# Kernel optimization log

Hardware: AMD Instinct MI355X
Metric: run time of the kernel (lower is better)

## Reference

```python
import jax, jax.numpy as jnp
import numpy as np

D = 1024      # model dim
DH = 64       # dim_head
H = 8         # heads
INNER = DH * H
L = 6         # depth
NL = 64       # num_latents
MF = 128      # max_num_frames
FF = 4 * D    # ff_mult * dim
B, T, F, V = 4, 8, 4, 256


def _ln(x, g, b):
    m = x.mean(-1, keepdims=True)
    v = x.var(-1, keepdims=True)
    return (x - m) / jnp.sqrt(v + 1e-5) * g + b


def setup_inputs() -> dict:
    key = jax.random.key(0)
    ks = jax.random.split(key, 8)
    s = 0.02
    x = jax.random.normal(ks[0], (B, T, F, V, D), jnp.float32)
    latents = jax.random.normal(ks[1], (NL, D), jnp.float32)
    frame_embs = jax.random.normal(ks[2], (MF, D), jnp.float32)
    Wq = jax.random.normal(ks[3], (L, D, INNER), jnp.float32) * s
    Wkv = jax.random.normal(ks[4], (L, D, 2 * INNER), jnp.float32) * s
    Wo = jax.random.normal(ks[5], (L, INNER, D), jnp.float32) * s
    W1 = jax.random.normal(ks[6], (L, D, FF), jnp.float32) * s
    W2 = jax.random.normal(ks[7], (L, FF, D), jnp.float32) * s
    ones = jnp.ones((L, D), jnp.float32)
    zeros = jnp.zeros((L, D), jnp.float32)
    return dict(
        x=x, latents=latents, frame_embs=frame_embs,
        g_media=ones, b_media=zeros, g_lat=ones, b_lat=zeros,
        Wq=Wq, Wkv=Wkv, Wo=Wo, g_ff=ones, b_ff=zeros, W1=W1, W2=W2,
        g_out=jnp.ones((D,), jnp.float32), b_out=jnp.zeros((D,), jnp.float32),
    )


def reference(x, latents, frame_embs, g_media, b_media, g_lat, b_lat,
              Wq, Wkv, Wo, g_ff, b_ff, W1, W2, g_out, b_out):
    scale = DH ** -0.5
    # add frame embeddings (indexed by T, as in original code), merge F,v dims
    x = x + frame_embs[:T][None, :, None, None, :]
    x = x.reshape(B, T, F * V, D)
    lat0 = jnp.broadcast_to(latents, (B, T, NL, D))

    def split_heads(a):  # (b, t, n, h*d) -> (b, h, t, n, d)
        return a.reshape(B, T, -1, H, DH).transpose(0, 3, 1, 2, 4)

    def block(lat, p):
        gm, bm, gl, bl, wq, wkv, wo, gf, bf, w1, w2 = p
        xm = _ln(x, gm, bm)
        ln_l = _ln(lat, gl, bl)
        q = (ln_l @ wq) * scale
        kv = jnp.concatenate([xm, ln_l], axis=-2) @ wkv
        k, v = jnp.split(kv, 2, axis=-1)
        q, k, v = split_heads(q), split_heads(k), split_heads(v)
        sim = jnp.einsum('bhtid,bhtjd->bhtij', q, k)
        attn = jax.nn.softmax(sim, axis=-1)
        o = jnp.einsum('bhtij,bhtjd->bhtid', attn, v)
        o = o.transpose(0, 2, 3, 1, 4).reshape(B, T, NL, INNER)
        lat = o @ wo + lat
        ff = jax.nn.gelu(_ln(lat, gf, bf) @ w1, approximate=False) @ w2
        return lat + ff, None

    lat, _ = jax.lax.scan(block, lat0,
                          (g_media, b_media, g_lat, b_lat, Wq, Wkv, Wo,
                           g_ff, b_ff, W1, W2))
    return _ln(lat, g_out, b_out)
```

## Files before the change

### kernel.cpp

```cpp
#include <hip/hip_runtime.h>
#include <math.h>

#define D_      1024
#define DH_     64
#define H_      8
#define INNER_  512
#define L_      6
#define NL_     64
#define FF_     4096
#define B_      4
#define T_      8
#define FV_     1024
#define BT_     32
#define MROWS_  32768
#define NKV_    1088
#define KVROWS_ 34816
#define ZB_     256

typedef __bf16 bf16;
typedef __bf16 bf16x8 __attribute__((ext_vector_type(8)));
typedef __bf16 bf16x4 __attribute__((ext_vector_type(4)));
typedef float  f32x4  __attribute__((ext_vector_type(4)));

#define BARRIER() { asm volatile("" ::: "memory"); __builtin_amdgcn_s_barrier(); asm volatile("" ::: "memory"); }
#define ENDPH() { __builtin_amdgcn_sched_barrier(0); asm volatile("s_waitcnt lgkmcnt(0)"); __builtin_amdgcn_sched_barrier(0); BARRIER(); }

__device__ __forceinline__ void gload_lds16(const bf16* g, bf16* l) {
    __builtin_amdgcn_global_load_lds(
        (const __attribute__((address_space(1))) unsigned int*)g,
        (__attribute__((address_space(3))) unsigned int*)l, 16, 0, 0);
}

__device__ __forceinline__ float wred_sum(float v) {
#pragma unroll
    for (int o = 32; o > 0; o >>= 1) v += __shfl_xor(v, o, 64);
    return v;
}

__device__ __forceinline__ float gelu_f(float x) {
    return 0.5f * x * (1.0f + erff(x * 0.70710678118654752440f));
}

__global__ __launch_bounds__(256) void xhat_k(const float* __restrict__ x,
                                              const float* __restrict__ fe,
                                              bf16* __restrict__ xhat) {
    __shared__ float red[8];
    int row = blockIdx.x;
    int t = (row >> 10) & 7;
    const float* xr = x + (size_t)row * D_;
    const float* fr_ = fe + (size_t)t * D_;
    int tid = threadIdx.x, c = tid * 4;
    float4 v = *(const float4*)(xr + c);
    float4 f = *(const float4*)(fr_ + c);
    v.x += f.x; v.y += f.y; v.z += f.z; v.w += f.w;
    float s = v.x + v.y + v.z + v.w;
    float ss = v.x * v.x + v.y * v.y + v.z * v.z + v.w * v.w;
    s = wred_sum(s); ss = wred_sum(ss);
    if ((tid & 63) == 0) { red[tid >> 6] = s; red[4 + (tid >> 6)] = ss; }
    __syncthreads();
    s = red[0] + red[1] + red[2] + red[3];
    ss = red[4] + red[5] + red[6] + red[7];
    float mean = s * (1.0f / D_);
    float rstd = rsqrtf(ss * (1.0f / D_) - mean * mean + 1e-5f);
    bf16x4 o;
    o[0] = (bf16)((v.x - mean) * rstd);
    o[1] = (bf16)((v.y - mean) * rstd);
    o[2] = (bf16)((v.z - mean) * rstd);
    o[3] = (bf16)((v.w - mean) * rstd);
    *(bf16x4*)(xhat + (size_t)row * D_ + c) = o;
}

__global__ __launch_bounds__(256) void latinit_k(const float* __restrict__ latents,
                                                 float* __restrict__ lat) {
    int row = blockIdx.x;
    int i = row & 63;
    int c = threadIdx.x * 4;
    float4 v = *(const float4*)(latents + (size_t)i * D_ + c);
    *(float4*)(lat + (size_t)row * D_ + c) = v;
}

template<int OUTF>
__global__ __launch_bounds__(256) void ln_k(const float* __restrict__ in,
                                            const float* __restrict__ g,
                                            const float* __restrict__ b,
                                            void* __restrict__ out) {
    __shared__ float red[8];
    int row = blockIdx.x;
    const float* x = in + (size_t)row * D_;
    int tid = threadIdx.x, c = tid * 4;
    float4 v = *(const float4*)(x + c);
    float s = v.x + v.y + v.z + v.w;
    float ss = v.x * v.x + v.y * v.y + v.z * v.z + v.w * v.w;
    s = wred_sum(s); ss = wred_sum(ss);
    if ((tid & 63) == 0) { red[tid >> 6] = s; red[4 + (tid >> 6)] = ss; }
    __syncthreads();
    s = red[0] + red[1] + red[2] + red[3];
    ss = red[4] + red[5] + red[6] + red[7];
    float mean = s * (1.0f / D_);
    float rstd = rsqrtf(ss * (1.0f / D_) - mean * mean + 1e-5f);
    float4 gv = *(const float4*)(g + c);
    float4 bv = *(const float4*)(b + c);
    float o0 = (v.x - mean) * rstd * gv.x + bv.x;
    float o1 = (v.y - mean) * rstd * gv.y + bv.y;
    float o2 = (v.z - mean) * rstd * gv.z + bv.z;
    float o3 = (v.w - mean) * rstd * gv.w + bv.w;
    if (OUTF) {
        *(float4*)((float*)out + (size_t)row * D_ + c) = make_float4(o0, o1, o2, o3);
    } else {
        bf16x4 o; o[0] = (bf16)o0; o[1] = (bf16)o1; o[2] = (bf16)o2; o[3] = (bf16)o3;
        *(bf16x4*)((bf16*)out + (size_t)row * D_ + c) = o;
    }
}

template<int NP, int OUTF>
__global__ __launch_bounds__(256) void accln_k(float* __restrict__ lat,
                                               const float* __restrict__ p, long long s,
                                               const float* __restrict__ g,
                                               const float* __restrict__ b,
                                               void* __restrict__ out) {
    __shared__ float red[8];
    int row = blockIdx.x;
    int tid = threadIdx.x, c = tid * 4;
    float* lr = lat + (size_t)row * D_;
    float4 a = *(const float4*)(lr + c);
#pragma unroll
    for (int w = 0; w < NP; w++) {
        float4 x = *(const float4*)(p + (size_t)w * s + (size_t)row * D_ + c);
        a.x += x.x; a.y += x.y; a.z += x.z; a.w += x.w;
    }
    if (!OUTF) *(float4*)(lr + c) = a;
    float sm = a.x + a.y + a.z + a.w;
    float ss = a.x * a.x + a.y * a.y + a.z * a.z + a.w * a.w;
    sm = wred_sum(sm); ss = wred_sum(ss);
    if ((tid & 63) == 0) { red[tid >> 6] = sm; red[4 + (tid >> 6)] = ss; }
    __syncthreads();
    sm = red[0] + red[1] + red[2] + red[3];
    ss = red[4] + red[5] + red[6] + red[7];
    float mean = sm * (1.0f / D_);
    float rstd = rsqrtf(ss * (1.0f / D_) - mean * mean + 1e-5f);
    float4 gv = *(const float4*)(g + c);
    float4 bv = *(const float4*)(b + c);
    float o0 = (a.x - mean) * rstd * gv.x + bv.x;
    float o1 = (a.y - mean) * rstd * gv.y + bv.y;
    float o2 = (a.z - mean) * rstd * gv.z + bv.z;
    float o3 = (a.w - mean) * rstd * gv.w + bv.w;
    if (OUTF) {
        *(float4*)((float*)out + (size_t)row * D_ + c) = make_float4(o0, o1, o2, o3);
    } else {
        bf16x4 o; o[0] = (bf16)o0; o[1] = (bf16)o1; o[2] = (bf16)o2; o[3] = (bf16)o3;
        *(bf16x4*)((bf16*)out + (size_t)row * D_ + c) = o;
    }
}

__device__ __forceinline__ void wt_tile(const float* __restrict__ in, int R, int C,
                                        bf16* __restrict__ out, int bx, int by,
                                        const float* __restrict__ sc,
                                        const float* __restrict__ bm,
                                        float* __restrict__ bkv) {
    __shared__ float t[32][33];
    int c0 = bx * 32, r0 = by * 32;
    int tx = threadIdx.x & 31, ty = threadIdx.x >> 5;
#pragma unroll
    for (int i = 0; i < 4; i++)
        t[ty + i * 8][tx] = in[(size_t)(r0 + ty + i * 8) * C + c0 + tx];
    __syncthreads();
    float scale = sc ? sc[r0 + tx] : 1.0f;
#pragma unroll
    for (int i = 0; i < 4; i++)
        out[(size_t)(c0 + ty + i * 8) * R + r0 + tx] = (bf16)(t[tx][ty + i * 8] * scale);
    if (bm && ty == 0) {
        float s = 0.0f;
#pragma unroll
        for (int r = 0; r < 32; r++) s += bm[r0 + r] * t[r][tx];
        atomicAdd(&bkv[c0 + tx], s);
    }
}

__global__ __launch_bounds__(256) void wprep_k(const float* __restrict__ wq,
                                               const float* __restrict__ wkv,
                                               const float* __restrict__ wo,
                                               const float* __restrict__ w1,
                                               const float* __restrict__ w2,
                                               const float* __restrict__ gm,
                                               const float* __restrict__ bm,
                                               float* __restrict__ bkv,
                                               bf16* __restrict__ BcatQ,
                                               bf16* __restrict__ BcatKV,
                                               bf16* __restrict__ WkvTg,
                                               bf16* __restrict__ WoT,
                                               bf16* __restrict__ W1T,
                                               bf16* __restrict__ W2T) {
    int id = blockIdx.x;
    if (id < 512)            wt_tile(wq, D_, INNER_, BcatQ, id & 15, id >> 4, nullptr, nullptr, nullptr);
    else if (id < 1536)  { int i = id - 512;  wt_tile(wkv, D_, 2 * INNER_, BcatKV, i & 31, i >> 5, nullptr, nullptr, nullptr); }
    else if (id < 2560)  { int i = id - 1536; wt_tile(wkv, D_, 2 * INNER_, WkvTg, i & 31, i >> 5, gm, bm, bkv); }
    else if (id < 3072)  { int i = id - 2560; wt_tile(wo, INNER_, D_, WoT, i & 31, i >> 5, nullptr, nullptr, nullptr); }
    else if (id < 7168)  { int i = id - 3072; wt_tile(w1, D_, FF_, W1T, i & 127, i >> 7, nullptr, nullptr, nullptr); }
    else                 { int i = id - 7168; wt_tile(w2, FF_, D_, W2T, i & 31, i >> 5, nullptr, nullptr, nullptr); }
}

__global__ __launch_bounds__(512, 1) void gemm_kv(const bf16* __restrict__ Ag,
                                                  const bf16* __restrict__ Bg,
                                                  bf16* __restrict__ KVb,
                                                  bf16* __restrict__ vt,
                                                  const float* __restrict__ bias) {
    __shared__ bf16 lds[2][32768];
    const int lda = D_, ldb = D_;
    const int tid = threadIdx.x;
    const int w = tid >> 6, lane = tid & 63;
    const int wm = w >> 2, wn = w & 3;
    const size_t m0 = (size_t)blockIdx.x * 256;
    const size_t n0 = (size_t)blockIdx.y * 256;
    const int nt = 16;

    const int p0 = (w * 2) * 64 + lane, p1 = p0 + 64;
    const int sr0 = p0 >> 3, sk0 = ((p0 & 7) ^ (sr0 & 7)) * 8;
    const int sr1 = p1 >> 3, sk1 = ((p1 & 7) ^ (sr1 & 7)) * 8;
    const int scw0 = (w * 2) * 512, scw1 = scw0 + 512;

    auto STAGE = [&](const bf16* g, int ld, size_t row0, int k0, bf16* bufb, int rb) {
        gload_lds16(g + (row0 + sr0) * (size_t)ld + k0 + sk0, bufb + rb + scw0);
        gload_lds16(g + (row0 + sr1) * (size_t)ld + k0 + sk1, bufb + rb + scw1);
    };

    const int fr = lane & 15;
    const int pK0 = (((lane >> 4)) ^ (fr & 7)) * 8;
    const int pK1 = ((4 + (lane >> 4)) ^ (fr & 7)) * 8;
    const size_t aoff = (size_t)(wm * 128 + fr) * 64;
    const size_t boff = 16384 + (size_t)(wn * 64 + fr) * 64;

    f32x4 acc[8][4];
#pragma unroll
    for (int i = 0; i < 8; i++)
#pragma unroll
        for (int j = 0; j < 4; j++)
#pragma unroll
            for (int r = 0; r < 4; r++) acc[i][j][r] = 0.0f;

    bf16x8 aX[4], aY[4], bA[4][2], bB[4][2];

    auto LDA2 = [&](const bf16* lb, int i0, bf16x8 (&d)[4]) {
        d[0] = *(const bf16x8*)(lb + aoff + (size_t)i0 * 1024 + pK0);
        d[1] = *(const bf16x8*)(lb + aoff + (size_t)i0 * 1024 + pK1);
        d[2] = *(const bf16x8*)(lb + aoff + (size_t)(i0 + 1) * 1024 + pK0);
        d[3] = *(const bf16x8*)(lb + aoff + (size_t)(i0 + 1) * 1024 + pK1);
    };
    auto LDB8 = [&](const bf16* lb, bf16x8 (&bb)[4][2]) {
#pragma unroll
        for (int j = 0; j < 4; j++) {
            bb[j][0] = *(const bf16x8*)(lb + boff + j * 1024 + pK0);
            bb[j][1] = *(const bf16x8*)(lb + boff + j * 1024 + pK1);
        }
    };
    auto MM2 = [&](int i0, bf16x8 (&a)[4], bf16x8 (&bb)[4][2]) {
        __builtin_amdgcn_s_setprio(1);
#pragma unroll
        for (int j = 0; j < 4; j++) {
            acc[i0][j]     = __builtin_amdgcn_mfma_f32_16x16x32_bf16(a[0], bb[j][0], acc[i0][j], 0, 0, 0);
            acc[i0][j]     = __builtin_amdgcn_mfma_f32_16x16x32_bf16(a[1], bb[j][1], acc[i0][j], 0, 0, 0);
            acc[i0 + 1][j] = __builtin_amdgcn_mfma_f32_16x16x32_bf16(a[2], bb[j][0], acc[i0 + 1][j], 0, 0, 0);
            acc[i0 + 1][j] = __builtin_amdgcn_mfma_f32_16x16x32_bf16(a[3], bb[j][1], acc[i0 + 1][j], 0, 0, 0);
        }
        __builtin_amdgcn_s_setprio(0);
    };

    STAGE(Bg, ldb, n0,       0, lds[0], 16384);
    STAGE(Bg, ldb, n0 + 128, 0, lds[0], 24576);
    STAGE(Ag, lda, m0,       0, lds[0], 0);
    STAGE(Ag, lda, m0 + 128, 0, lds[0], 8192);
    STAGE(Bg, ldb, n0,       64, lds[1], 16384);
    STAGE(Bg, ldb, n0 + 128, 64, lds[1], 24576);
    STAGE(Ag, lda, m0,       64, lds[1], 0);
    asm volatile("s_waitcnt vmcnt(6)");
    BARRIER();
    LDB8(lds[0], bA);
    LDA2(lds[0], 0, aX);

    auto tile4 = [&](const bf16* lb, bf16* lbn, bf16x8 (&BU)[4][2], bf16x8 (&BL)[4][2], int t) {
        bf16* lbw = (bf16*)lb;
        LDA2(lb, 2, aY);
        if (t + 1 < nt) STAGE(Ag, lda, m0 + 128, (t + 1) << 6, lbn, 8192);
        MM2(0, aX, BU);
        ENDPH();
        LDA2(lb, 4, aX);
        if (t + 2 < nt) STAGE(Bg, ldb, n0, (t + 2) << 6, lbw, 16384);
        MM2(2, aY, BU);
        ENDPH();
        LDA2(lb, 6, aY);
        if (t + 2 < nt) STAGE(Bg, ldb, n0 + 128, (t + 2) << 6, lbw, 24576);
        MM2(4, aX, BU);
        __builtin_amdgcn_sched_barrier(0);
        asm volatile("s_waitcnt lgkmcnt(0)");
        __builtin_amdgcn_sched_barrier(0);
        if (t < nt - 2)       { asm volatile("s_waitcnt vmcnt(4)"); }
        else if (t == nt - 2) { asm volatile("s_waitcnt vmcnt(0)"); }
        BARRIER();
        if (t + 1 < nt) { LDB8(lbn, BL); LDA2(lbn, 0, aX); }
        if (t + 2 < nt) STAGE(Ag, lda, m0, (t + 2) << 6, lbw, 0);
        MM2(6, aY, BU);
        ENDPH();
    };

    for (int t = 0; t < nt; t += 2) {
        tile4(lds[0], lds[1], bA, bB, t);
        tile4(lds[1], lds[0], bB, bA, t + 1);
    }

    const int fq = (lane >> 4) * 4;
#pragma unroll
    for (int i = 0; i < 8; i++)
#pragma unroll
        for (int j = 0; j < 4; j++) {
            size_t cb = n0 + wn * 64 + j * 16 + fr;
            float bv = bias[cb];
            size_t mb = m0 + wm * 128 + i * 16 + fq;
            if (cb < 512) {
#pragma unroll
                for (int r = 0; r < 4; r++) {
                    size_t m = mb + r;
                    size_t rb = m + ((m >> 10) << 6);
                    KVb[rb * 512 + cb] = (bf16)(acc[i][j][r] + bv);
                }
            } else {
                int hh = ((int)cb - 512) >> 6, dh = ((int)cb - 512) & 63;
                size_t bt = mb >> 10, jl = mb & 1023;
                bf16x4 v4;
#pragma unroll
                for (int r = 0; r < 4; r++) v4[r] = (bf16)(acc[i][j][r] + bv);
                *(bf16x4*)(vt + ((bt * 8 + hh) * 64 + dh) * (size_t)NKV_ + jl) = v4;
            }
        }
}

template<int MODE>
__global__ __launch_bounds__(512, 1) void gemm_ff(const bf16* __restrict__ Ag, int lda,
                                                  const bf16* __restrict__ Bg, int ldb,
                                                  void* __restrict__ C, int ldc,
                                                  int K, long long czs) {
    __shared__ bf16 lds[2][24576];
    const int tid = threadIdx.x;
    const int w = tid >> 6, lane = tid & 63;
    const int wm = w >> 2, wn = w & 3;
    const size_t m0 = (size_t)blockIdx.x * 128;
    const size_t n0 = (size_t)blockIdx.y * 256;
    const int klen = K / gridDim.z;
    const int koff = blockIdx.z * klen;
    const int nt = klen >> 6;

    const int p0 = (w * 2) * 64 + lane, p1 = p0 + 64;
    const int sr0 = p0 >> 3, sk0 = ((p0 & 7) ^ (sr0 & 7)) * 8;
    const int sr1 = p1 >> 3, sk1 = ((p1 & 7) ^ (sr1 & 7)) * 8;
    const int scw0 = (w * 2) * 512, scw1 = scw0 + 512;

    auto STAGE = [&](const bf16* g, int ld, size_t row0, int k0, bf16* bufb, int rb) {
        gload_lds16(g + (row0 + sr0) * (size_t)ld + k0 + sk0, bufb + rb + scw0);
        gload_lds16(g + (row0 + sr1) * (size_t)ld + k0 + sk1, bufb + rb + scw1);
    };

    const int fr = lane & 15;
    const int pK0 = (((lane >> 4)) ^ (fr & 7)) * 8;
    const int pK1 = ((4 + (lane >> 4)) ^ (fr & 7)) * 8;
    const size_t aoff = (size_t)(wm * 64 + fr) * 64;
    const size_t boff = 8192 + (size_t)(wn * 64 + fr) * 64;

    f32x4 acc[4][4];
#pragma unroll
    for (int i = 0; i < 4; i++)
#pragma unroll
        for (int j = 0; j < 4; j++)
#pragma unroll
            for (int r = 0; r < 4; r++) acc[i][j][r] = 0.0f;

    bf16x8 aX[2], aY[2], bA[4][2], bB[4][2];

    auto LDA1 = [&](const bf16* lb, int i0, bf16x8 (&d)[2]) {
        d[0] = *(const bf16x8*)(lb + aoff + (size_t)i0 * 1024 + pK0);
        d[1] = *(const bf16x8*)(lb + aoff + (size_t)i0 * 1024 + pK1);
    };
    auto LDB8 = [&](const bf16* lb, bf16x8 (&bb)[4][2]) {
#pragma unroll
        for (int j = 0; j < 4; j++) {
            bb[j][0] = *(const bf16x8*)(lb + boff + j * 1024 + pK0);
            bb[j][1] = *(const bf16x8*)(lb + boff + j * 1024 + pK1);
        }
    };
    auto MM1 = [&](int i0, bf16x8 (&a)[2], bf16x8 (&bb)[4][2]) {
        __builtin_amdgcn_s_setprio(1);
#pragma unroll
        for (int j = 0; j < 4; j++) {
            acc[i0][j] = __builtin_amdgcn_mfma_f32_16x16x32_bf16(a[0], bb[j][0], acc[i0][j], 0, 0, 0);
            acc[i0][j] = __builtin_amdgcn_mfma_f32_16x16x32_bf16(a[1], bb[j][1], acc[i0][j], 0, 0, 0);
        }
        __builtin_amdgcn_s_setprio(0);
    };

    STAGE(Ag, lda, m0,       koff,      lds[0], 0);
    STAGE(Bg, ldb, n0,       koff,      lds[0], 8192);
    STAGE(Bg, ldb, n0 + 128, koff,      lds[0], 16384);
    STAGE(Bg, ldb, n0,       koff + 64, lds[1], 8192);
    STAGE(Bg, ldb, n0 + 128, koff + 64, lds[1], 16384);
    asm volatile("s_waitcnt vmcnt(4)");
    BARRIER();
    LDB8(lds[0], bA);
    LDA1(lds[0], 0, aX);

    auto tile4 = [&](const bf16* lb, bf16* lbn, bf16x8 (&BU)[4][2], bf16x8 (&BL)[4][2], int t) {
        bf16* lbw = (bf16*)lb;
        LDA1(lb, 1, aY);
        if (t + 1 < nt) STAGE(Ag, lda, m0, koff + ((t + 1) << 6), lbn, 0);
        MM1(0, aX, BU);
        ENDPH();
        LDA1(lb, 2, aX);
        if (t + 2 < nt) STAGE(Bg, ldb, n0, koff + ((t + 2) << 6), lbw, 8192);
        MM1(1, aY, BU);
        ENDPH();
        LDA1(lb, 3, aY);
        if (t + 2 < nt) STAGE(Bg, ldb, n0 + 128, koff + ((t + 2) << 6), lbw, 16384);
        MM1(2, aX, BU);
        __builtin_amdgcn_sched_barrier(0);
        asm volatile("s_waitcnt lgkmcnt(0)");
        __builtin_amdgcn_sched_barrier(0);
        if (t < nt - 2)       { asm volatile("s_waitcnt vmcnt(4)"); }
        else if (t == nt - 2) { asm volatile("s_waitcnt vmcnt(0)"); }
        BARRIER();
        if (t + 1 < nt) { LDB8(lbn, BL); LDA1(lbn, 0, aX); }
        MM1(3, aY, BU);
        ENDPH();
    };

    for (int t = 0; t < nt; t += 2) {
        tile4(lds[0], lds[1], bA, bB, t);
        tile4(lds[1], lds[0], bB, bA, t + 1);
    }

    const int fq = (lane >> 4) * 4;
#pragma unroll
    for (int i = 0; i < 4; i++)
#pragma unroll
        for (int j = 0; j < 4; j++) {
            size_t cb = n0 + wn * 64 + j * 16 + fr;
            size_t mb = m0 + wm * 64 + i * 16 + fq;
#pragma unroll
            for (int r = 0; r < 4; r++) {
                float v = acc[i][j][r];
                if (MODE == 4) {
                    ((float*)C + blockIdx.z * czs)[(mb + r) * (size_t)ldc + cb] = v;
                } else {
                    ((bf16*)C)[(mb + r) * (size_t)ldc + cb] = (bf16)gelu_f(v);
                }
            }
        }
}

template<int MODE, int CMAP>
__global__ __launch_bounds__(256) void gemm128(const bf16* __restrict__ A, int lda,
                                               const bf16* __restrict__ Bw, int ldb,
                                               void* __restrict__ C, int ldc,
                                               int K, float scale,
                                               long long czs, void* __restrict__ C2,
                                               void* __restrict__ C3) {
    __shared__ bf16 As[128 * 32];
    __shared__ bf16 Bs[128 * 32];
    const int tid = threadIdx.x;
    const int wave = tid >> 6;
    const int lane = tid & 63;
    const size_t m0 = (size_t)blockIdx.x * 128;
    const size_t n0 = (size_t)blockIdx.y * 128;
    const int wm = (wave >> 1) * 64;
    const int wn = (wave & 1) * 64;

    const int klen = K / gridDim.z;
    const int koff = blockIdx.z * klen;

    const int r0 = tid >> 2;
    const int c0 = ((tid & 3) ^ ((tid >> 3) & 3)) * 8;
    const bf16* ga0 = A + (m0 + r0) * lda + c0 + koff;
    const bf16* ga1 = A + (m0 + r0 + 64) * lda + c0 + koff;
    const bf16* gb0 = Bw + (n0 + r0) * ldb + c0 + koff;
    const bf16* gb1 = Bw + (n0 + r0 + 64) * ldb + c0 + koff;
    bf16* la0 = As + wave * 512;
    bf16* la1 = As + 2048 + wave * 512;
    bf16* lb0 = Bs + wave * 512;
    bf16* lb1 = Bs + 2048 + wave * 512;

    f32x4 acc[4][4];
#pragma unroll
    for (int i = 0; i < 4; i++)
#pragma unroll
        for (int j = 0; j < 4; j++)
#pragma unroll
            for (int r = 0; r < 4; r++) acc[i][j][r] = 0.0f;

    const int fr = lane & 15;
    const int q = lane >> 4;
    const int sw = (q ^ ((fr >> 1) & 3)) * 8;

    for (int kt = 0; kt < klen; kt += 32) {
        gload_lds16(ga0 + kt, la0);
        gload_lds16(ga1 + kt, la1);
        gload_lds16(gb0 + kt, lb0);
        gload_lds16(gb1 + kt, lb1);
        __syncthreads();
        bf16x8 af[4], bfv[4];
#pragma unroll
        for (int i = 0; i < 4; i++) {
            af[i]  = *(const bf16x8*)(As + (wm + i * 16 + fr) * 32 + sw);
            bfv[i] = *(const bf16x8*)(Bs + (wn + i * 16 + fr) * 32 + sw);
        }
#pragma unroll
        for (int i = 0; i < 4; i++)
#pragma unroll
            for (int j = 0; j < 4; j++)
                acc[i][j] = __builtin_amdgcn_mfma_f32_16x16x32_bf16(af[i], bfv[j], acc[i][j], 0, 0, 0);
        __syncthreads();
    }

    const int fq = (lane >> 4) * 4;
#pragma unroll
    for (int i = 0; i < 4; i++)
#pragma unroll
        for (int j = 0; j < 4; j++) {
            size_t cb = n0 + wn + j * 16 + fr;
            size_t mb = m0 + wm + i * 16 + fq;
            if (CMAP == 3) {
                if (cb < 512) {
#pragma unroll
                    for (int r = 0; r < 4; r++)
                        ((bf16*)C)[(mb + r) * 512 + cb] = (bf16)(acc[i][j][r] * scale);
                } else if (cb < 1024) {
#pragma unroll
                    for (int r = 0; r < 4; r++) {
                        size_t m = mb + r;
                        size_t rb = (m >> 6) * (size_t)NKV_ + 1024 + (m & 63);
                        ((bf16*)C2)[rb * 512 + (cb - 512)] = (bf16)acc[i][j][r];
                    }
                } else {
                    int hh = ((int)cb - 1024) >> 6, dh = ((int)cb - 1024) & 63;
                    size_t bt = mb >> 6, jl = 1024 + (mb & 63);
                    bf16x4 v4;
#pragma unroll
                    for (int r = 0; r < 4; r++) v4[r] = (bf16)acc[i][j][r];
                    *(bf16x4*)((bf16*)C3 + ((bt * 8 + hh) * 64 + dh) * (size_t)NKV_ + jl) = v4;
                }
            } else {
#pragma unroll
                for (int r = 0; r < 4; r++) {
                    float v = acc[i][j][r];
                    if (MODE == 4) {
                        ((float*)C + blockIdx.z * czs)[(mb + r) * ldc + cb] = v;
                    } else {
                        ((bf16*)C)[(mb + r) * ldc + cb] = (bf16)v;
                    }
                }
            }
        }
}

__global__ __launch_bounds__(256, 2) void attn_k(const bf16* __restrict__ qb,
                                                 const bf16* __restrict__ KVb,
                                                 const bf16* __restrict__ vt,
                                                 bf16* __restrict__ ob) {
    __shared__ float comb[4][64 * 66];
    __shared__ float sc[4][64];
    __shared__ float mw[4][64], lw[4][64];
    const int z = blockIdx.x, bt = z >> 3, h = z & 7;
    const int tid = threadIdx.x, w = tid >> 6, lane = tid & 63;
    const int fr = lane & 15, g = lane >> 4;
    const bf16* Qz = qb + (size_t)(bt * 64) * INNER_ + h * DH_;
    const bf16* Kz = KVb + (size_t)bt * NKV_ * 512 + h * DH_;
    const bf16* Vz = vt + (size_t)z * (DH_ * NKV_);
    bf16* Pw = (bf16*)(&comb[w][0]);

    bf16x8 qf[4][2];
#pragma unroll
    for (int nj = 0; nj < 4; nj++)
#pragma unroll
        for (int ks = 0; ks < 2; ks++)
            qf[nj][ks] = *(const bf16x8*)(Qz + (size_t)(fr + 16 * nj) * INNER_ + g * 8 + ks * 32);

    f32x4 acc_o[4][4];
#pragma unroll
    for (int i = 0; i < 4; i++)
#pragma unroll
        for (int j = 0; j < 4; j++)
#pragma unroll
            for (int r = 0; r < 4; r++) acc_o[i][j][r] = 0.0f;
    float m_reg[4] = {-INFINITY, -INFINITY, -INFINITY, -INFINITY};
    float l_reg[4] = {0.0f, 0.0f, 0.0f, 0.0f};

    const int nch = (w == 0) ? 5 : 4;
    for (int ci = 0; ci < nch; ci++) {
        const int kc0 = (w + ci * 4) * 64;
        f32x4 s[4][4];
#pragma unroll
        for (int i = 0; i < 4; i++)
#pragma unroll
            for (int j = 0; j < 4; j++)
#pragma unroll
                for (int r = 0; r < 4; r++) s[i][j][r] = 0.0f;
#pragma unroll
        for (int ks = 0; ks < 2; ks++) {
            bf16x8 kf[4];
#pragma unroll
            for (int mi = 0; mi < 4; mi++)
                kf[mi] = *(const bf16x8*)(Kz + (size_t)(kc0 + fr + 16 * mi) * 512 + g * 8 + ks * 32);
#pragma unroll
            for (int mi = 0; mi < 4; mi++)
#pragma unroll
                for (int nj = 0; nj < 4; nj++)
                    s[mi][nj] = __builtin_amdgcn_mfma_f32_16x16x32_bf16(kf[mi], qf[nj][ks], s[mi][nj], 0, 0, 0);
        }
        float pmax[4];
#pragma unroll
        for (int nj = 0; nj < 4; nj++) {
            float mx = s[0][nj][0];
#pragma unroll
            for (int mi = 0; mi < 4; mi++)
#pragma unroll
                for (int r = 0; r < 4; r++) mx = fmaxf(mx, s[mi][nj][r]);
            mx = fmaxf(mx, __shfl_xor(mx, 16, 64));
            mx = fmaxf(mx, __shfl_xor(mx, 32, 64));
            pmax[nj] = mx;
        }
        bool grew = (pmax[0] > m_reg[0]) || (pmax[1] > m_reg[1]) ||
                    (pmax[2] > m_reg[2]) || (pmax[3] > m_reg[3]);
        if (__any(grew ? 1 : 0)) {
            float so[4];
#pragma unroll
            for (int nj = 0; nj < 4; nj++) {
                float mn = fmaxf(m_reg[nj], pmax[nj]);
                so[nj] = __expf(m_reg[nj] - mn);
                m_reg[nj] = mn;
                l_reg[nj] *= so[nj];
            }
            if (g == 0) {
#pragma unroll
                for (int nj = 0; nj < 4; nj++) sc[w][fr + 16 * nj] = so[nj];
            }
            asm volatile("s_waitcnt lgkmcnt(0)" ::: "memory");
#pragma unroll
            for (int mi = 0; mi < 4; mi++)
#pragma unroll
                for (int r = 0; r < 4; r++) {
                    float sq = sc[w][16 * mi + 4 * g + r];
#pragma unroll
                    for (int jd = 0; jd < 4; jd++) acc_o[mi][jd][r] *= sq;
                }
        }
        float psum[4] = {0.0f, 0.0f, 0.0f, 0.0f};
#pragma unroll
        for (int mi = 0; mi < 4; mi++)
#pragma unroll
            for (int nj = 0; nj < 4; nj++) {
                bf16x4 pb4;
#pragma unroll
                for (int r = 0; r < 4; r++) {
                    float pv = __expf(s[mi][nj][r] - m_reg[nj]);
                    psum[nj] += pv;
                    pb4[r] = (bf16)pv;
                }
                *(bf16x4*)(Pw + (size_t)(fr + 16 * nj) * 72 + 16 * mi + 4 * g) = pb4;
            }
#pragma unroll
        for (int nj = 0; nj < 4; nj++) {
            float ps = psum[nj];
            ps += __shfl_xor(ps, 16, 64);
            ps += __shfl_xor(ps, 32, 64);
            l_reg[nj] += ps;
        }
        asm volatile("s_waitcnt lgkmcnt(0)" ::: "memory");
#pragma unroll
        for (int ks = 0; ks < 2; ks++) {
            bf16x8 af[4], vf[4];
#pragma unroll
            for (int mi = 0; mi < 4; mi++)
                af[mi] = *(const bf16x8*)(Pw + (size_t)(fr + 16 * mi) * 72 + g * 8 + ks * 32);
#pragma unroll
            for (int jd = 0; jd < 4; jd++)
                vf[jd] = *(const bf16x8*)(Vz + (size_t)(fr + 16 * jd) * NKV_ + kc0 + g * 8 + ks * 32);
#pragma unroll
            for (int mi = 0; mi < 4; mi++)
#pragma unroll
                for (int jd = 0; jd < 4; jd++)
                    acc_o[mi][jd] = __builtin_amdgcn_mfma_f32_16x16x32_bf16(af[mi], vf[jd], acc_o[mi][jd], 0, 0, 0);
        }
    }

    if (g == 0) {
#pragma unroll
        for (int nj = 0; nj < 4; nj++) {
            mw[w][fr + 16 * nj] = m_reg[nj];
            lw[w][fr + 16 * nj] = l_reg[nj];
        }
    }
    asm volatile("s_waitcnt lgkmcnt(0)" ::: "memory");
#pragma unroll
    for (int mi = 0; mi < 4; mi++)
#pragma unroll
        for (int jd = 0; jd < 4; jd++)
#pragma unroll
            for (int r = 0; r < 4; r++)
                comb[w][(16 * mi + 4 * g + r) * 66 + fr + 16 * jd] = acc_o[mi][jd][r];
    __syncthreads();
    {
        int q = tid >> 2, d0 = (tid & 3) * 16;
        float M = fmaxf(fmaxf(mw[0][q], mw[1][q]), fmaxf(mw[2][q], mw[3][q]));
        float al[4], l = 0.0f;
#pragma unroll
        for (int ww = 0; ww < 4; ww++) { al[ww] = __expf(mw[ww][q] - M); l += al[ww] * lw[ww][q]; }
        float inv = 1.0f / l;
        bf16 outv[16];
#pragma unroll
        for (int dd = 0; dd < 16; dd++) {
            float o = 0.0f;
#pragma unroll
            for (int ww = 0; ww < 4; ww++) o += comb[ww][q * 66 + d0 + dd] * al[ww];
            outv[dd] = (bf16)(o * inv);
        }
        bf16* dst = ob + (size_t)(bt * 64 + q) * INNER_ + h * 64 + d0;
        *(bf16x8*)dst = *(bf16x8*)outv;
        *(bf16x8*)(dst + 8) = *(bf16x8*)(outv + 8);
    }
}

extern "C" void kernel_launch(void* const* d_in, const int* in_sizes, int n_in,
                              void* d_out, int out_size, void* d_ws, size_t ws_size,
                              hipStream_t stream) {
    const float* x       = (const float*)d_in[0];
    const float* latents = (const float*)d_in[1];
    const float* fe      = (const float*)d_in[2];
    const float* g_media = (const float*)d_in[3];
    const float* b_media = (const float*)d_in[4];
    const float* g_lat   = (const float*)d_in[5];
    const float* b_lat   = (const float*)d_in[6];
    const float* Wq      = (const float*)d_in[7];
    const float* Wkv     = (const float*)d_in[8];
    const float* Wo      = (const float*)d_in[9];
    const float* g_ff    = (const float*)d_in[10];
    const float* b_ff    = (const float*)d_in[11];
    const float* W1      = (const float*)d_in[12];
    const float* W2      = (const float*)d_in[13];
    const float* g_out   = (const float*)d_in[14];
    const float* b_out   = (const float*)d_in[15];

    char* p = (char*)d_ws;
    auto alloc = [&](size_t bytes) { char* r = p; p += (bytes + 255) & ~(size_t)255; return r; };
    bf16*  xhat = (bf16*)alloc((size_t)MROWS_ * D_ * 2);
    float* lat  = (float*)alloc((size_t)2048 * D_ * 4);
    bf16*  lnl  = (bf16*)alloc((size_t)2048 * D_ * 2);
    bf16*  qb   = (bf16*)alloc((size_t)2048 * INNER_ * 2);
    bf16*  KVb  = (bf16*)alloc((size_t)KVROWS_ * 512 * 2);
    bf16*  vt   = (bf16*)alloc((size_t)ZB_ * DH_ * NKV_ * 2);
    bf16*  ob   = (bf16*)alloc((size_t)2048 * INNER_ * 2);
    bf16*  Bcat = (bf16*)alloc((size_t)1536 * D_ * 2);
    bf16*  WkvTg= (bf16*)alloc((size_t)D_ * D_ * 2);
    bf16*  WoT  = (bf16*)alloc((size_t)D_ * INNER_ * 2);
    bf16*  W1T  = (bf16*)alloc((size_t)FF_ * D_ * 2);
    bf16*  W2T  = (bf16*)alloc((size_t)D_ * FF_ * 2);
    float* bkv  = (float*)alloc(1024 * 4);
    float* ffp  = (float*)alloc((size_t)4 * 2048 * D_ * 4);
    bf16*  ffh  = vt;

    xhat_k<<<MROWS_, 256, 0, stream>>>(x, fe, xhat);
    latinit_k<<<2048, 256, 0, stream>>>(latents, lat);
    ln_k<0><<<2048, 256, 0, stream>>>(lat, g_lat, b_lat, lnl);

    const long long PS = (long long)2048 * D_;

    for (int l = 0; l < L_; l++) {
        const float* gm = g_media + (size_t)l * D_;
        const float* bm = b_media + (size_t)l * D_;
        const float* gf = g_ff + (size_t)l * D_;
        const float* bf_ = b_ff + (size_t)l * D_;
        const float* wq = Wq + (size_t)l * D_ * INNER_;
        const float* wkv = Wkv + (size_t)l * D_ * 2 * INNER_;
        const float* wo = Wo + (size_t)l * INNER_ * D_;
        const float* w1 = W1 + (size_t)l * D_ * FF_;
        const float* w2 = W2 + (size_t)l * FF_ * D_;

        hipMemsetAsync(bkv, 0, 1024 * 4, stream);
        wprep_k<<<11264, 256, 0, stream>>>(wq, wkv, wo, w1, w2, gm, bm, bkv,
                                           Bcat, Bcat + (size_t)512 * D_, WkvTg, WoT, W1T, W2T);

        gemm_kv<<<dim3(128, 4), 512, 0, stream>>>(xhat, WkvTg, KVb, vt, bkv);
        gemm128<0, 3><<<dim3(16, 12), 256, 0, stream>>>(
            lnl, D_, Bcat, D_, qb, 0, D_, 0.125f, 0, KVb, vt);

        attn_k<<<ZB_, 256, 0, stream>>>(qb, KVb, vt, ob);

        gemm128<4, 0><<<dim3(16, 8, 2), 256, 0, stream>>>(
            ob, INNER_, WoT, INNER_, ffp, D_, INNER_, 1.0f, PS, nullptr, nullptr);
        accln_k<2, 0><<<2048, 256, 0, stream>>>(lat, ffp, PS, gf, bf_, lnl);

        gemm_ff<3><<<dim3(16, 16), 512, 0, stream>>>(
            lnl, D_, W1T, D_, ffh, FF_, D_, 0);
        gemm_ff<4><<<dim3(16, 4, 4), 512, 0, stream>>>(
            ffh, FF_, W2T, FF_, ffp, D_, FF_, PS);
        if (l < L_ - 1) {
            accln_k<4, 0><<<2048, 256, 0, stream>>>(lat, ffp, PS,
                g_lat + (size_t)(l + 1) * D_, b_lat + (size_t)(l + 1) * D_, lnl);
        } else {
            accln_k<4, 1><<<2048, 256, 0, stream>>>(lat, ffp, PS, g_out, b_out, (float*)d_out);
        }
    }
}
```

Measured before the change: 1.324 ms.

## Replace register-prefetched GEMM main loop with per-phase barrier-synchronized schedule

```diff
diff --git a/kernel.cpp b/kernel.cpp
--- a/kernel.cpp
+++ b/kernel.cpp
@@ -237,33 +237,6 @@
 #pragma unroll
             for (int r = 0; r < 4; r++) acc[i][j][r] = 0.0f;
 
-    bf16x8 aX[4], aY[4], bA[4][2], bB[4][2];
-
-    auto LDA2 = [&](const bf16* lb, int i0, bf16x8 (&d)[4]) {
-        d[0] = *(const bf16x8*)(lb + aoff + (size_t)i0 * 1024 + pK0);
-        d[1] = *(const bf16x8*)(lb + aoff + (size_t)i0 * 1024 + pK1);
-        d[2] = *(const bf16x8*)(lb + aoff + (size_t)(i0 + 1) * 1024 + pK0);
-        d[3] = *(const bf16x8*)(lb + aoff + (size_t)(i0 + 1) * 1024 + pK1);
-    };
-    auto LDB8 = [&](const bf16* lb, bf16x8 (&bb)[4][2]) {
-#pragma unroll
-        for (int j = 0; j < 4; j++) {
-            bb[j][0] = *(const bf16x8*)(lb + boff + j * 1024 + pK0);
-            bb[j][1] = *(const bf16x8*)(lb + boff + j * 1024 + pK1);
-        }
-    };
-    auto MM2 = [&](int i0, bf16x8 (&a)[4], bf16x8 (&bb)[4][2]) {
-        __builtin_amdgcn_s_setprio(1);
-#pragma unroll
-        for (int j = 0; j < 4; j++) {
-            acc[i0][j]     = __builtin_amdgcn_mfma_f32_16x16x32_bf16(a[0], bb[j][0], acc[i0][j], 0, 0, 0);
-            acc[i0][j]     = __builtin_amdgcn_mfma_f32_16x16x32_bf16(a[1], bb[j][1], acc[i0][j], 0, 0, 0);
-            acc[i0 + 1][j] = __builtin_amdgcn_mfma_f32_16x16x32_bf16(a[2], bb[j][0], acc[i0 + 1][j], 0, 0, 0);
-            acc[i0 + 1][j] = __builtin_amdgcn_mfma_f32_16x16x32_bf16(a[3], bb[j][1], acc[i0 + 1][j], 0, 0, 0);
-        }
-        __builtin_amdgcn_s_setprio(0);
-    };
-
     STAGE(Bg, ldb, n0,       0, lds[0], 16384);
     STAGE(Bg, ldb, n0 + 128, 0, lds[0], 24576);
     STAGE(Ag, lda, m0,       0, lds[0], 0);
@@ -273,37 +246,97 @@
     STAGE(Ag, lda, m0,       64, lds[1], 0);
     asm volatile("s_waitcnt vmcnt(6)");
     BARRIER();
-    LDB8(lds[0], bA);
-    LDA2(lds[0], 0, aX);
-
-    auto tile4 = [&](const bf16* lb, bf16* lbn, bf16x8 (&BU)[4][2], bf16x8 (&BL)[4][2], int t) {
-        bf16* lbw = (bf16*)lb;
-        LDA2(lb, 2, aY);
-        if (t + 1 < nt) STAGE(Ag, lda, m0 + 128, (t + 1) << 6, lbn, 8192);
-        MM2(0, aX, BU);
-        ENDPH();
-        LDA2(lb, 4, aX);
-        if (t + 2 < nt) STAGE(Bg, ldb, n0, (t + 2) << 6, lbw, 16384);
-        MM2(2, aY, BU);
-        ENDPH();
-        LDA2(lb, 6, aY);
-        if (t + 2 < nt) STAGE(Bg, ldb, n0 + 128, (t + 2) << 6, lbw, 24576);
-        MM2(4, aX, BU);
-        __builtin_amdgcn_sched_barrier(0);
-        asm volatile("s_waitcnt lgkmcnt(0)");
-        __builtin_amdgcn_sched_barrier(0);
-        if (t < nt - 2)       { asm volatile("s_waitcnt vmcnt(4)"); }
-        else if (t == nt - 2) { asm volatile("s_waitcnt vmcnt(0)"); }
-        BARRIER();
-        if (t + 1 < nt) { LDB8(lbn, BL); LDA2(lbn, 0, aX); }
-        if (t + 2 < nt) STAGE(Ag, lda, m0, (t + 2) << 6, lbw, 0);
-        MM2(6, aY, BU);
-        ENDPH();
-    };
-
-    for (int t = 0; t < nt; t += 2) {
-        tile4(lds[0], lds[1], bA, bB, t);
-        tile4(lds[1], lds[0], bB, bA, t + 1);
+
+    for (int t = 0; t < nt; ++t) {
+        const bf16* lb = lds[t & 1];
+        bf16* lbw = lds[t & 1];
+        bf16* lbn = lds[(t + 1) & 1];
+        const int kt1 = (t + 1) << 6, kt2 = (t + 2) << 6;
+        bf16x8 bfr[4][2];
+
+        {
+#pragma unroll
+            for (int j = 0; j < 4; j++) {
+                bfr[j][0] = *(const bf16x8*)(lb + boff + j * 1024 + pK0);
+                bfr[j][1] = *(const bf16x8*)(lb + boff + j * 1024 + pK1);
+            }
+            bf16x8 a00 = *(const bf16x8*)(lb + aoff + 0 * 1024 + pK0);
+            bf16x8 a01 = *(const bf16x8*)(lb + aoff + 0 * 1024 + pK1);
+            bf16x8 a10 = *(const bf16x8*)(lb + aoff + 1 * 1024 + pK0);
+            bf16x8 a11 = *(const bf16x8*)(lb + aoff + 1 * 1024 + pK1);
+            if (t + 1 < nt) STAGE(Ag, lda, m0 + 128, kt1, lbn, 8192);
+            BARRIER();
+            asm volatile("s_waitcnt lgkmcnt(0)");
+            __builtin_amdgcn_s_setprio(1);
+#pragma unroll
+            for (int j = 0; j < 4; j++) {
+                acc[0][j] = __builtin_amdgcn_mfma_f32_16x16x32_bf16(a00, bfr[j][0], acc[0][j], 0, 0, 0);
+                acc[0][j] = __builtin_amdgcn_mfma_f32_16x16x32_bf16(a01, bfr[j][1], acc[0][j], 0, 0, 0);
+                acc[1][j] = __builtin_amdgcn_mfma_f32_16x16x32_bf16(a10, bfr[j][0], acc[1][j], 0, 0, 0);
+                acc[1][j] = __builtin_amdgcn_mfma_f32_16x16x32_bf16(a11, bfr[j][1], acc[1][j], 0, 0, 0);
+            }
+            __builtin_amdgcn_s_setprio(0);
+            BARRIER();
+        }
+        {
+            bf16x8 a00 = *(const bf16x8*)(lb + aoff + 2 * 1024 + pK0);
+            bf16x8 a01 = *(const bf16x8*)(lb + aoff + 2 * 1024 + pK1);
+            bf16x8 a10 = *(const bf16x8*)(lb + aoff + 3 * 1024 + pK0);
+            bf16x8 a11 = *(const bf16x8*)(lb + aoff + 3 * 1024 + pK1);
+            if (t + 2 < nt) STAGE(Bg, ldb, n0, kt2, lbw, 16384);
+            BARRIER();
+            asm volatile("s_waitcnt lgkmcnt(0)");
+            __builtin_amdgcn_s_setprio(1);
+#pragma unroll
+            for (int j = 0; j < 4; j++) {
+                acc[2][j] = __builtin_amdgcn_mfma_f32_16x16x32_bf16(a00, bfr[j][0], acc[2][j], 0, 0, 0);
+                acc[2][j] = __builtin_amdgcn_mfma_f32_16x16x32_bf16(a01, bfr[j][1], acc[2][j], 0, 0, 0);
+                acc[3][j] = __builtin_amdgcn_mfma_f32_16x16x32_bf16(a10, bfr[j][0], acc[3][j], 0, 0, 0);
+                acc[3][j] = __builtin_amdgcn_mfma_f32_16x16x32_bf16(a11, bfr[j][1], acc[3][j], 0, 0, 0);
+            }
+            __builtin_amdgcn_s_setprio(0);
+            BARRIER();
+        }
+        {
+            bf16x8 a00 = *(const bf16x8*)(lb + aoff + 4 * 1024 + pK0);
+            bf16x8 a01 = *(const bf16x8*)(lb + aoff + 4 * 1024 + pK1);
+            bf16x8 a10 = *(const bf16x8*)(lb + aoff + 5 * 1024 + pK0);
+            bf16x8 a11 = *(const bf16x8*)(lb + aoff + 5 * 1024 + pK1);
+            if (t + 2 < nt) STAGE(Bg, ldb, n0 + 128, kt2, lbw, 24576);
+            BARRIER();
+            asm volatile("s_waitcnt lgkmcnt(0)");
+            __builtin_amdgcn_s_setprio(1);
+#pragma unroll
+            for (int j = 0; j < 4; j++) {
+                acc[4][j] = __builtin_amdgcn_mfma_f32_16x16x32_bf16(a00, bfr[j][0], acc[4][j], 0, 0, 0);
+                acc[4][j] = __builtin_amdgcn_mfma_f32_16x16x32_bf16(a01, bfr[j][1], acc[4][j], 0, 0, 0);
+                acc[5][j] = __builtin_amdgcn_mfma_f32_16x16x32_bf16(a10, bfr[j][0], acc[5][j], 0, 0, 0);
+                acc[5][j] = __builtin_amdgcn_mfma_f32_16x16x32_bf16(a11, bfr[j][1], acc[5][j], 0, 0, 0);
+            }
+            __builtin_amdgcn_s_setprio(0);
+            BARRIER();
+        }
+        {
+            bf16x8 a00 = *(const bf16x8*)(lb + aoff + 6 * 1024 + pK0);
+            bf16x8 a01 = *(const bf16x8*)(lb + aoff + 6 * 1024 + pK1);
+            bf16x8 a10 = *(const bf16x8*)(lb + aoff + 7 * 1024 + pK0);
+            bf16x8 a11 = *(const bf16x8*)(lb + aoff + 7 * 1024 + pK1);
+            if (t + 2 < nt) STAGE(Ag, lda, m0, kt2, lbw, 0);
+            BARRIER();
+            asm volatile("s_waitcnt lgkmcnt(0)");
+            __builtin_amdgcn_s_setprio(1);
+#pragma unroll
+            for (int j = 0; j < 4; j++) {
+                acc[6][j] = __builtin_amdgcn_mfma_f32_16x16x32_bf16(a00, bfr[j][0], acc[6][j], 0, 0, 0);
+                acc[6][j] = __builtin_amdgcn_mfma_f32_16x16x32_bf16(a01, bfr[j][1], acc[6][j], 0, 0, 0);
+                acc[7][j] = __builtin_amdgcn_mfma_f32_16x16x32_bf16(a10, bfr[j][0], acc[7][j], 0, 0, 0);
+                acc[7][j] = __builtin_amdgcn_mfma_f32_16x16x32_bf16(a11, bfr[j][1], acc[7][j], 0, 0, 0);
+            }
+            __builtin_amdgcn_s_setprio(0);
+            if (t < nt - 2)       { asm volatile("s_waitcnt vmcnt(6)"); }
+            else if (t == nt - 2) { asm volatile("s_waitcnt vmcnt(0)"); }
+            BARRIER();
+        }
     }
 
     const int fq = (lane >> 4) * 4;
```

Measured after the change: 1.280 ms. 3.4% less time.
